# Optimization experiments

Measured on AMD Instinct MI355X. Metric: run time of the kernel, lower is better.

The kernel has to match this reference:

```python
import jax, jax.numpy as jnp
import numpy as np

N = 100000
E = 1600000
IN_C = 128
OUT_C = 64
HID = 2 * OUT_C  # 128


def setup_inputs() -> dict:
    key = jax.random.key(0)
    ks = jax.random.split(key, 10)
    s = lambda fan_in: 1.0 / np.sqrt(fan_in)
    inp = {
        "x": jax.random.normal(ks[0], (N, IN_C), dtype=jnp.float32),
        "edge_index": jax.random.randint(ks[1], (2, E), 0, N, dtype=jnp.int64),
        # SAGEConv params: lin_l acts on aggregated neighbors (with bias), lin_r on root (no bias)
        "W1l": jax.random.uniform(ks[2], (IN_C, HID), jnp.float32, -s(IN_C), s(IN_C)),
        "b1": jnp.zeros((HID,), jnp.float32),
        "W1r": jax.random.uniform(ks[3], (IN_C, HID), jnp.float32, -s(IN_C), s(IN_C)),
        "Wml": jax.random.uniform(ks[4], (HID, OUT_C), jnp.float32, -s(HID), s(HID)),
        "bm": jnp.zeros((OUT_C,), jnp.float32),
        "Wmr": jax.random.uniform(ks[5], (HID, OUT_C), jnp.float32, -s(HID), s(HID)),
        "Wsl": jax.random.uniform(ks[6], (HID, OUT_C), jnp.float32, -s(HID), s(HID)),
        "bs": jnp.zeros((OUT_C,), jnp.float32),
        "Wsr": jax.random.uniform(ks[7], (HID, OUT_C), jnp.float32, -s(HID), s(HID)),
    }
    return inp


def _sage_mean(x, src, dst, Wl, b, Wr):
    n = x.shape[0]
    # mean aggregation of source features onto destination nodes
    agg = jax.ops.segment_sum(x[src], dst, num_segments=n)
    cnt = jax.ops.segment_sum(jnp.ones((src.shape[0],), x.dtype), dst, num_segments=n)
    agg = agg / jnp.maximum(cnt, 1.0)[:, None]
    return agg @ Wl + b + x @ Wr


def reference(x, edge_index, W1l, b1, W1r, Wml, bm, Wmr, Wsl, bs, Wsr):
    src, dst = edge_index[0], edge_index[1]
    h = jax.nn.relu(_sage_mean(x, src, dst, W1l, b1, W1r))
    mu = _sage_mean(h, src, dst, Wml, bm, Wmr)
    logstd = _sage_mean(h, src, dst, Wsl, bs, Wsr)
    return mu, logstd
```

## Files before the change

### kernel.cpp

```cpp
#include <hip/hip_runtime.h>


typedef __attribute__((ext_vector_type(8))) short bf16x8;
typedef __attribute__((ext_vector_type(4))) float f32x4;
typedef __attribute__((ext_vector_type(2))) float f32x2;

#define SHIFT 9
#define BW 512

__device__ __forceinline__ unsigned short f2bf(float f) {
    unsigned u = __builtin_bit_cast(unsigned, f);
    u += 0x7fff + ((u >> 16) & 1);
    return (unsigned short)(u >> 16);
}
__device__ __forceinline__ float bflo(unsigned u) { return __builtin_bit_cast(float, u << 16); }
__device__ __forceinline__ float bfhi(unsigned u) { return __builtin_bit_cast(float, u & 0xffff0000u); }

__global__ __launch_bounds__(256) void stage1_kernel(
    const float* __restrict__ x, const int* __restrict__ raw,
    const float* __restrict__ W1l, const float* __restrict__ W1r,
    const float* __restrict__ Wml, const float* __restrict__ Wmr,
    const float* __restrict__ Wsl, const float* __restrict__ Wsr,
    const float* __restrict__ bm, const float* __restrict__ bs,
    unsigned short* __restrict__ B1p, unsigned short* __restrict__ B2p,
    float* __restrict__ bc, unsigned short* __restrict__ A1,
    unsigned short* __restrict__ A2, int* __restrict__ bcnt,
    unsigned* __restrict__ recs, int n, int nE, int cap, int nBinA, int nXB) {
    const int b = blockIdx.x;
    const int t = threadIdx.x;
    if (b < nBinA) {
        __shared__ int cnt[256];
        __shared__ int cur[256];
        __shared__ int gbase[256];
        __shared__ int sflag;
        const int e0 = b * 4096;
        const int e1 = (e0 + 4096 < nE) ? e0 + 4096 : nE;
        int acc = 0;
        for (int e = e0 + t; e < e1; e += 256) acc |= raw[2 * e + 1];
        if (t == 0) sflag = 0;
        cnt[t] = 0;
        cur[t] = 0;
        __syncthreads();
        if (acc) atomicOr(&sflag, 1);
        __syncthreads();
        const bool is64 = (sflag == 0);
        for (int e = e0 + t; e < e1; e += 256) {
            int d = is64 ? raw[2 * (nE + e)] : raw[nE + e];
            atomicAdd(&cnt[d >> SHIFT], 1);
        }
        __syncthreads();
        gbase[t] = cnt[t] ? atomicAdd(&bcnt[t], cnt[t]) : 0;
        __syncthreads();
        for (int e = e0 + t; e < e1; e += 256) {
            int s, d;
            if (is64) { s = raw[2 * e]; d = raw[2 * (nE + e)]; }
            else      { s = raw[e];     d = raw[nE + e]; }
            int bk = d >> SHIFT;
            int pos = gbase[bk] + atomicAdd(&cur[bk], 1);
            if (pos < cap)
                recs[(size_t)bk * cap + pos] = ((unsigned)s << SHIFT) | (unsigned)(d & (BW - 1));
        }
    } else if (b < nBinA + nXB) {
        int i = ((b - nBinA) * 256 + t) * 4;
        if (i < n * 128) {
            float4 v = *reinterpret_cast<const float4*>(x + i);
            int row = i >> 7, col = i & 127;
            unsigned short* p = A1 + (size_t)row * 256 + 128 + col;
            p[0] = f2bf(v.x); p[1] = f2bf(v.y); p[2] = f2bf(v.z); p[3] = f2bf(v.w);
        }
    } else if (b < nBinA + nXB + 128) {
        int i = (b - nBinA - nXB) * 256 + t;
        int j = i & 7, lq = (i >> 3) & 63, ks = (i >> 9) & 7, nf = i >> 12;
        int k = ks * 32 + (lq >> 4) * 8 + j;
        int c = nf * 16 + (lq & 15);
        float w1 = (k < 128) ? W1l[k * 128 + c] : W1r[(k - 128) * 128 + c];
        float w2;
        if (k < 128) w2 = (c < 64) ? Wml[k * 64 + c] : Wsl[k * 64 + (c - 64)];
        else         w2 = (c < 64) ? Wmr[(k - 128) * 64 + c] : Wsr[(k - 128) * 64 + (c - 64)];
        B1p[i] = f2bf(w1);
        B2p[i] = f2bf(w2);
        if (i < 128) bc[i] = (i < 64) ? bm[i] : bs[i - 64];
    } else {
        if (t < 64) {
            ((unsigned*)A1)[(size_t)n * 128 + 64 + t] = 0;
            ((unsigned*)A2)[(size_t)n * 128 + 64 + t] = 0;
        }
    }
}

__global__ __launch_bounds__(256) void binB_kernel(
    const unsigned* __restrict__ recs, const int* __restrict__ bcnt,
    int* __restrict__ rowptrP, int* __restrict__ cnts,
    int* __restrict__ csr, int cap, int n, int NB) {
    __shared__ int sdeg[BW];
    __shared__ int scur[BW];
    __shared__ int ssum[256];
    const int b = blockIdx.x;
    const int t = threadIdx.x;
    const int node0 = b << SHIFT;

    int rawb = (t < NB) ? bcnt[t] : 0;
    ssum[t] = rawb;
    __syncthreads();
    for (int off = 1; off < 256; off <<= 1) {
        int val = (t >= off) ? ssum[t - off] : 0;
        __syncthreads();
        ssum[t] += val;
        __syncthreads();
    }
    const int base = ((b == 0) ? 0 : ssum[b - 1]) + b * 3 * BW;
    int cnt = bcnt[b];
    if (cnt > cap) cnt = cap;
    const unsigned* r = recs + (size_t)b * cap;
    __syncthreads();

    sdeg[t] = 0;
    sdeg[t + 256] = 0;
    __syncthreads();
    for (int i = t; i < cnt; i += 256) atomicAdd(&sdeg[r[i] & (BW - 1)], 1);
    __syncthreads();
    int d0 = sdeg[2 * t], d1 = sdeg[2 * t + 1];
    int p0 = (d0 + 3) & ~3, p1 = (d1 + 3) & ~3;
    int sum = p0 + p1;
    ssum[t] = sum;
    __syncthreads();
    for (int off = 1; off < 256; off <<= 1) {
        int val = (t >= off) ? ssum[t - off] : 0;
        __syncthreads();
        ssum[t] += val;
        __syncthreads();
    }
    int ex = ssum[t] - sum;
    scur[2 * t] = ex;
    scur[2 * t + 1] = ex + p0;
    __syncthreads();
#pragma unroll
    for (int q = 0; q < 2; ++q) {
        int i = 2 * t + q;
        int node = node0 + i;
        if (node < n) {
            rowptrP[node] = base + scur[i];
            cnts[node] = sdeg[i];
        }
    }
    __syncthreads();
    for (int i = t; i < cnt; i += 256) {
        unsigned rec = r[i];
        int pos = base + atomicAdd(&scur[rec & (BW - 1)], 1);
        csr[pos] = (int)(rec >> SHIFT);
    }
    __syncthreads();
#pragma unroll
    for (int q = 0; q < 2; ++q) {
        int i = 2 * t + q;
        int node = node0 + i;
        if (node < n) {
            int d = sdeg[i];
            int pad = (4 - (d & 3)) & 3;
            int st = base + scur[i];
            for (int k = 0; k < pad; ++k) csr[st + k] = n;
        }
    }
}

__global__ __launch_bounds__(256) void gather_kernel(const unsigned int* __restrict__ feat,
                                                     const int* __restrict__ rowptrP,
                                                     const int* __restrict__ cnts,
                                                     const int* __restrict__ csr,
                                                     unsigned int* __restrict__ agg, int n) {
    int wv = (blockIdx.x * 256 + threadIdx.x) >> 6;
    if (wv >= n) return;
    int lane = threadIdx.x & 63;
    int eg = lane >> 4;
    int c4 = (lane & 15) * 4;
    int beg = rowptrP[wv];
    int deg = cnts[wv];
    int endp = beg + ((deg + 3) & ~3);
    f32x2 a0 = (f32x2)(0.f), a1 = (f32x2)(0.f), a2 = (f32x2)(0.f), a3 = (f32x2)(0.f);
    if (deg > 0) {
        int s0 = csr[beg + eg];
        uint4 v = *reinterpret_cast<const uint4*>(feat + (size_t)s0 * 128 + c4);
        int nx = beg + 4;
        int s1 = csr[(nx < endp ? nx : beg) + eg];
        while (nx < endp) {
            uint4 v2 = *reinterpret_cast<const uint4*>(feat + (size_t)s1 * 128 + c4);
            int nx2 = nx + 4;
            int s2 = csr[(nx2 < endp ? nx2 : beg) + eg];
            a0 += (f32x2){bflo(v.x), bfhi(v.x)};
            a1 += (f32x2){bflo(v.y), bfhi(v.y)};
            a2 += (f32x2){bflo(v.z), bfhi(v.z)};
            a3 += (f32x2){bflo(v.w), bfhi(v.w)};
            v = v2;
            s1 = s2;
            nx = nx2;
        }
        a0 += (f32x2){bflo(v.x), bfhi(v.x)};
        a1 += (f32x2){bflo(v.y), bfhi(v.y)};
        a2 += (f32x2){bflo(v.z), bfhi(v.z)};
        a3 += (f32x2){bflo(v.w), bfhi(v.w)};
    }
    float acc[8] = {a0.x, a0.y, a1.x, a1.y, a2.x, a2.y, a3.x, a3.y};
#pragma unroll
    for (int q = 0; q < 8; ++q) {
        acc[q] += __shfl_xor(acc[q], 16);
        acc[q] += __shfl_xor(acc[q], 32);
    }
    if (eg == 0) {
        float ic = 1.0f / fmaxf((float)deg, 1.0f);
        uint4 r;
        r.x = (unsigned)f2bf(acc[0] * ic) | ((unsigned)f2bf(acc[1] * ic) << 16);
        r.y = (unsigned)f2bf(acc[2] * ic) | ((unsigned)f2bf(acc[3] * ic) << 16);
        r.z = (unsigned)f2bf(acc[4] * ic) | ((unsigned)f2bf(acc[5] * ic) << 16);
        r.w = (unsigned)f2bf(acc[6] * ic) | ((unsigned)f2bf(acc[7] * ic) << 16);
        *reinterpret_cast<uint4*>(agg + (size_t)wv * 128 + c4) = r;
    }
}

template <int MODE>
__global__ __launch_bounds__(256) void mfma_gemm(const unsigned short* __restrict__ A,
                                                 const unsigned short* __restrict__ Bp,
                                                 const float* __restrict__ bias,
                                                 void* __restrict__ outp, int n) {
    const int tid = threadIdx.x;
    const int w = tid >> 6, l = tid & 63;
    const int lr = l & 15;
    const int lg = l >> 4;
    const int row0 = blockIdx.x * 128 + w * 32;

    f32x4 acc[2][8];
#pragma unroll
    for (int mf = 0; mf < 2; ++mf)
#pragma unroll
        for (int nf = 0; nf < 8; ++nf) acc[mf][nf] = (f32x4)(0.0f);

    int r0 = row0 + lr;       if (r0 > n - 1) r0 = n - 1;
    int r1 = row0 + 16 + lr;  if (r1 > n - 1) r1 = n - 1;
    const unsigned short* a0p = A + (size_t)r0 * 256 + lg * 8;
    const unsigned short* a1p = A + (size_t)r1 * 256 + lg * 8;
    const unsigned short* bp = Bp + (size_t)l * 8;

    for (int ks = 0; ks < 8; ++ks) {
        bf16x8 a0 = *reinterpret_cast<const bf16x8*>(a0p + ks * 32);
        bf16x8 a1 = *reinterpret_cast<const bf16x8*>(a1p + ks * 32);
#pragma unroll
        for (int nf = 0; nf < 8; ++nf) {
            bf16x8 b = *reinterpret_cast<const bf16x8*>(bp + ((nf * 8 + ks) << 9));
            acc[0][nf] = __builtin_amdgcn_mfma_f32_16x16x32_bf16(a0, b, acc[0][nf], 0, 0, 0);
            acc[1][nf] = __builtin_amdgcn_mfma_f32_16x16x32_bf16(a1, b, acc[1][nf], 0, 0, 0);
        }
    }

    float bv[8];
#pragma unroll
    for (int nf = 0; nf < 8; ++nf) bv[nf] = bias[nf * 16 + lr];

#pragma unroll
    for (int mf = 0; mf < 2; ++mf)
#pragma unroll
        for (int j = 0; j < 4; ++j) {
            int row = row0 + mf * 16 + lg * 4 + j;
            if (row >= n) continue;
#pragma unroll
            for (int nf = 0; nf < 8; ++nf) {
                int col = nf * 16 + lr;
                float v = acc[mf][nf][j] + bv[nf];
                if (MODE == 0) {
                    v = fmaxf(v, 0.0f);
                    ((unsigned short*)outp)[(size_t)row * 256 + 128 + col] = f2bf(v);
                } else {
                    float* o = (float*)outp;
                    if (col < 64) o[(size_t)row * 64 + col] = v;
                    else o[(size_t)n * 64 + (size_t)row * 64 + (col - 64)] = v;
                }
            }
        }
}

extern "C" void kernel_launch(void* const* d_in, const int* in_sizes, int n_in,
                              void* d_out, int out_size, void* d_ws, size_t ws_size,
                              hipStream_t stream) {
    const float* x = (const float*)d_in[0];
    const int* eidx_raw = (const int*)d_in[1];
    const float* W1l = (const float*)d_in[2];
    const float* b1 = (const float*)d_in[3];
    const float* W1r = (const float*)d_in[4];
    const float* Wml = (const float*)d_in[5];
    const float* bm = (const float*)d_in[6];
    const float* Wmr = (const float*)d_in[7];
    const float* Wsl = (const float*)d_in[8];
    const float* bs = (const float*)d_in[9];
    const float* Wsr = (const float*)d_in[10];
    float* out = (float*)d_out;

    const int n = in_sizes[0] / 128;
    const int nE = in_sizes[1] / 2;

    const int NB = ((n - 1) >> SHIFT) + 1;
    long long capll = (((long long)nE << SHIFT) / n) * 5 / 4 + 1024;
    const int cap = (int)((capll + 15) & ~15LL);
    const int csr_ints = nE + NB * 3 * BW + 64;

    char* ws = (char*)d_ws;
    const size_t a_bytes = (size_t)(n + 1) * 512;
    const size_t a1_off = 0;
    const size_t a2_off = a1_off + a_bytes;
    const size_t recs_off = a2_off;
    const size_t csr_off = a2_off + a_bytes;
    const size_t rowptr_off = csr_off + (size_t)csr_ints * 4;
    const size_t cnts_off = rowptr_off + (size_t)n * 4;
    const size_t bcnt_off = cnts_off + (size_t)n * 4;
    const size_t b1p_off = (bcnt_off + 1024 + 255) & ~(size_t)255;
    const size_t b2p_off = b1p_off + 65536;
    const size_t bc_off = b2p_off + 65536;

    unsigned short* A1 = (unsigned short*)(ws + a1_off);
    unsigned short* A2 = (unsigned short*)(ws + a2_off);
    unsigned* recs = (unsigned*)(ws + recs_off);
    int* csr = (int*)(ws + csr_off);
    int* rowptrP = (int*)(ws + rowptr_off);
    int* cnts = (int*)(ws + cnts_off);
    int* bcnt = (int*)(ws + bcnt_off);
    unsigned short* B1p = (unsigned short*)(ws + b1p_off);
    unsigned short* B2p = (unsigned short*)(ws + b2p_off);
    float* bc = (float*)(ws + bc_off);

    hipMemsetAsync(bcnt, 0, 1024, stream);

    const int nBinA = (nE + 4095) / 4096;
    const int nXB = (n * 32 + 255) / 256;
    stage1_kernel<<<nBinA + nXB + 129, 256, 0, stream>>>(
        x, eidx_raw, W1l, W1r, Wml, Wmr, Wsl, Wsr, bm, bs,
        B1p, B2p, bc, A1, A2, bcnt, recs, n, nE, cap, nBinA, nXB);

    binB_kernel<<<NB, 256, 0, stream>>>(recs, bcnt, rowptrP, cnts, csr, cap, n, NB);

    const int gather_blocks = (n * 64 + 255) / 256;
    const int gemm_blocks = (n + 127) / 128;

    gather_kernel<<<gather_blocks, 256, 0, stream>>>(
        (const unsigned int*)A1 + 64, rowptrP, cnts, csr, (unsigned int*)A1, n);
    mfma_gemm<0><<<gemm_blocks, 256, 0, stream>>>(A1, B1p, b1, A2, n);

    gather_kernel<<<gather_blocks, 256, 0, stream>>>(
        (const unsigned int*)A2 + 64, rowptrP, cnts, csr, (unsigned int*)A2, n);
    mfma_gemm<1><<<gemm_blocks, 256, 0, stream>>>(A2, B2p, bc, out, n);
}
```

Before: 269.0 us.

## Fuse neighbor gather into MFMA GEMM via LDS-staged aggregate tile

Each GEMM block now computes the mean aggregation for its own 128 rows and stores it in a swizzled LDS tile. The MFMA loop reads the aggregated half of A from LDS and the root-feature half from a compact bf16 feature array, so the aggregate no longer makes a round trip through global memory and two launches are dropped. The bucket width is halved to 256 nodes with up to 512 buckets, which doubles the binning tables. In exchange, the gather now runs with far fewer waves in flight per node (one wave walks 32 nodes serially), which may hurt latency hiding on the irregular loads.

```diff
diff --git a/kernel.cpp b/kernel.cpp
--- a/kernel.cpp
+++ b/kernel.cpp
@@ -5,8 +5,9 @@
 typedef __attribute__((ext_vector_type(4))) float f32x4;
 typedef __attribute__((ext_vector_type(2))) float f32x2;
 
-#define SHIFT 9
-#define BW 512
+#define SHIFT 8
+#define BW 256
+#define NBMAX 512
 
 __device__ __forceinline__ unsigned short f2bf(float f) {
     unsigned u = __builtin_bit_cast(unsigned, f);
@@ -23,23 +24,23 @@
     const float* __restrict__ Wsl, const float* __restrict__ Wsr,
     const float* __restrict__ bm, const float* __restrict__ bs,
     unsigned short* __restrict__ B1p, unsigned short* __restrict__ B2p,
-    float* __restrict__ bc, unsigned short* __restrict__ A1,
-    unsigned short* __restrict__ A2, int* __restrict__ bcnt,
+    float* __restrict__ bc, unsigned short* __restrict__ X16,
+    unsigned short* __restrict__ H16, int* __restrict__ bcnt,
     unsigned* __restrict__ recs, int n, int nE, int cap, int nBinA, int nXB) {
     const int b = blockIdx.x;
     const int t = threadIdx.x;
     if (b < nBinA) {
-        __shared__ int cnt[256];
-        __shared__ int cur[256];
-        __shared__ int gbase[256];
+        __shared__ int cnt[NBMAX];
+        __shared__ int cur[NBMAX];
+        __shared__ int gbase[NBMAX];
         __shared__ int sflag;
         const int e0 = b * 4096;
         const int e1 = (e0 + 4096 < nE) ? e0 + 4096 : nE;
         int acc = 0;
         for (int e = e0 + t; e < e1; e += 256) acc |= raw[2 * e + 1];
         if (t == 0) sflag = 0;
-        cnt[t] = 0;
-        cur[t] = 0;
+        cnt[t] = 0; cnt[t + 256] = 0;
+        cur[t] = 0; cur[t + 256] = 0;
         __syncthreads();
         if (acc) atomicOr(&sflag, 1);
         __syncthreads();
@@ -50,6 +51,7 @@
         }
         __syncthreads();
         gbase[t] = cnt[t] ? atomicAdd(&bcnt[t], cnt[t]) : 0;
+        gbase[t + 256] = cnt[t + 256] ? atomicAdd(&bcnt[t + 256], cnt[t + 256]) : 0;
         __syncthreads();
         for (int e = e0 + t; e < e1; e += 256) {
             int s, d;
@@ -65,7 +67,7 @@
         if (i < n * 128) {
             float4 v = *reinterpret_cast<const float4*>(x + i);
             int row = i >> 7, col = i & 127;
-            unsigned short* p = A1 + (size_t)row * 256 + 128 + col;
+            unsigned short* p = X16 + (size_t)row * 128 + col;
             p[0] = f2bf(v.x); p[1] = f2bf(v.y); p[2] = f2bf(v.z); p[3] = f2bf(v.w);
         }
     } else if (b < nBinA + nXB + 128) {
@@ -82,8 +84,8 @@
         if (i < 128) bc[i] = (i < 64) ? bm[i] : bs[i - 64];
     } else {
         if (t < 64) {
-            ((unsigned*)A1)[(size_t)n * 128 + 64 + t] = 0;
-            ((unsigned*)A2)[(size_t)n * 128 + 64 + t] = 0;
+            ((unsigned*)X16)[(size_t)n * 64 + t] = 0;
+            ((unsigned*)H16)[(size_t)n * 64 + t] = 0;
         }
     }
 }
@@ -94,54 +96,51 @@
     int* __restrict__ csr, int cap, int n, int NB) {
     __shared__ int sdeg[BW];
     __shared__ int scur[BW];
-    __shared__ int ssum[256];
+    __shared__ int sscan[256];
+    __shared__ int sb[NBMAX];
     const int b = blockIdx.x;
     const int t = threadIdx.x;
-    const int node0 = b << SHIFT;
-
-    int rawb = (t < NB) ? bcnt[t] : 0;
-    ssum[t] = rawb;
+
+    int v0 = (2 * t < NB) ? bcnt[2 * t] : 0;
+    int v1 = (2 * t + 1 < NB) ? bcnt[2 * t + 1] : 0;
+    int sum = v0 + v1;
+    sscan[t] = sum;
     __syncthreads();
     for (int off = 1; off < 256; off <<= 1) {
-        int val = (t >= off) ? ssum[t - off] : 0;
-        __syncthreads();
-        ssum[t] += val;
-        __syncthreads();
-    }
-    const int base = ((b == 0) ? 0 : ssum[b - 1]) + b * 3 * BW;
+        int val = (t >= off) ? sscan[t - off] : 0;
+        __syncthreads();
+        sscan[t] += val;
+        __syncthreads();
+    }
+    int ex = sscan[t] - sum;
+    sb[2 * t] = ex;
+    sb[2 * t + 1] = ex + v0;
+    __syncthreads();
+    const int base = sb[b] + b * 3 * BW;
     int cnt = bcnt[b];
     if (cnt > cap) cnt = cap;
     const unsigned* r = recs + (size_t)b * cap;
-    __syncthreads();
 
     sdeg[t] = 0;
-    sdeg[t + 256] = 0;
     __syncthreads();
     for (int i = t; i < cnt; i += 256) atomicAdd(&sdeg[r[i] & (BW - 1)], 1);
     __syncthreads();
-    int d0 = sdeg[2 * t], d1 = sdeg[2 * t + 1];
-    int p0 = (d0 + 3) & ~3, p1 = (d1 + 3) & ~3;
-    int sum = p0 + p1;
-    ssum[t] = sum;
+    int d = sdeg[t];
+    int p = (d + 3) & ~3;
+    sscan[t] = p;
     __syncthreads();
     for (int off = 1; off < 256; off <<= 1) {
-        int val = (t >= off) ? ssum[t - off] : 0;
-        __syncthreads();
-        ssum[t] += val;
-        __syncthreads();
-    }
-    int ex = ssum[t] - sum;
-    scur[2 * t] = ex;
-    scur[2 * t + 1] = ex + p0;
-    __syncthreads();
-#pragma unroll
-    for (int q = 0; q < 2; ++q) {
-        int i = 2 * t + q;
-        int node = node0 + i;
-        if (node < n) {
-            rowptrP[node] = base + scur[i];
-            cnts[node] = sdeg[i];
-        }
+        int val = (t >= off) ? sscan[t - off] : 0;
+        __syncthreads();
+        sscan[t] += val;
+        __syncthreads();
+    }
+    int exn = sscan[t] - p;
+    scur[t] = exn;
+    const int node = (b << SHIFT) + t;
+    if (node < n) {
+        rowptrP[node] = base + exn;
+        cnts[node] = d;
     }
     __syncthreads();
     for (int i = t; i < cnt; i += 256) {
@@ -150,79 +149,71 @@
         csr[pos] = (int)(rec >> SHIFT);
     }
     __syncthreads();
-#pragma unroll
-    for (int q = 0; q < 2; ++q) {
-        int i = 2 * t + q;
-        int node = node0 + i;
-        if (node < n) {
-            int d = sdeg[i];
-            int pad = (4 - (d & 3)) & 3;
-            int st = base + scur[i];
-            for (int k = 0; k < pad; ++k) csr[st + k] = n;
-        }
-    }
-}
-
-__global__ __launch_bounds__(256) void gather_kernel(const unsigned int* __restrict__ feat,
-                                                     const int* __restrict__ rowptrP,
-                                                     const int* __restrict__ cnts,
-                                                     const int* __restrict__ csr,
-                                                     unsigned int* __restrict__ agg, int n) {
-    int wv = (blockIdx.x * 256 + threadIdx.x) >> 6;
-    if (wv >= n) return;
-    int lane = threadIdx.x & 63;
-    int eg = lane >> 4;
-    int c4 = (lane & 15) * 4;
-    int beg = rowptrP[wv];
-    int deg = cnts[wv];
-    int endp = beg + ((deg + 3) & ~3);
-    f32x2 a0 = (f32x2)(0.f), a1 = (f32x2)(0.f), a2 = (f32x2)(0.f), a3 = (f32x2)(0.f);
-    if (deg > 0) {
-        int s0 = csr[beg + eg];
-        uint4 v = *reinterpret_cast<const uint4*>(feat + (size_t)s0 * 128 + c4);
-        int nx = beg + 4;
-        int s1 = csr[(nx < endp ? nx : beg) + eg];
-        while (nx < endp) {
-            uint4 v2 = *reinterpret_cast<const uint4*>(feat + (size_t)s1 * 128 + c4);
-            int nx2 = nx + 4;
-            int s2 = csr[(nx2 < endp ? nx2 : beg) + eg];
-            a0 += (f32x2){bflo(v.x), bfhi(v.x)};
-            a1 += (f32x2){bflo(v.y), bfhi(v.y)};
-            a2 += (f32x2){bflo(v.z), bfhi(v.z)};
-            a3 += (f32x2){bflo(v.w), bfhi(v.w)};
-            v = v2;
-            s1 = s2;
-            nx = nx2;
-        }
-        a0 += (f32x2){bflo(v.x), bfhi(v.x)};
-        a1 += (f32x2){bflo(v.y), bfhi(v.y)};
-        a2 += (f32x2){bflo(v.z), bfhi(v.z)};
-        a3 += (f32x2){bflo(v.w), bfhi(v.w)};
-    }
-    float acc[8] = {a0.x, a0.y, a1.x, a1.y, a2.x, a2.y, a3.x, a3.y};
-#pragma unroll
-    for (int q = 0; q < 8; ++q) {
-        acc[q] += __shfl_xor(acc[q], 16);
-        acc[q] += __shfl_xor(acc[q], 32);
-    }
-    if (eg == 0) {
-        float ic = 1.0f / fmaxf((float)deg, 1.0f);
-        uint4 r;
-        r.x = (unsigned)f2bf(acc[0] * ic) | ((unsigned)f2bf(acc[1] * ic) << 16);
-        r.y = (unsigned)f2bf(acc[2] * ic) | ((unsigned)f2bf(acc[3] * ic) << 16);
-        r.z = (unsigned)f2bf(acc[4] * ic) | ((unsigned)f2bf(acc[5] * ic) << 16);
-        r.w = (unsigned)f2bf(acc[6] * ic) | ((unsigned)f2bf(acc[7] * ic) << 16);
-        *reinterpret_cast<uint4*>(agg + (size_t)wv * 128 + c4) = r;
+    if (node < n) {
+        int pad = (4 - (d & 3)) & 3;
+        int st = base + scur[t];
+        for (int k = 0; k < pad; ++k) csr[st + k] = n;
     }
 }
 
 template <int MODE>
-__global__ __launch_bounds__(256) void mfma_gemm(const unsigned short* __restrict__ A,
-                                                 const unsigned short* __restrict__ Bp,
-                                                 const float* __restrict__ bias,
-                                                 void* __restrict__ outp, int n) {
+__global__ __launch_bounds__(256) void gg_kernel(
+    const unsigned short* __restrict__ feat,
+    const int* __restrict__ rowptrP, const int* __restrict__ cnts,
+    const int* __restrict__ csr, const unsigned short* __restrict__ Bp,
+    const float* __restrict__ bias, void* __restrict__ outp, int n) {
+    __shared__ __align__(16) unsigned aggT[128 * 64];
     const int tid = threadIdx.x;
     const int w = tid >> 6, l = tid & 63;
+    const unsigned* featU = (const unsigned*)feat;
+
+    {
+        const int eg = l >> 4;
+        const int c4u = (l & 15) * 4;
+        const int nodeBase = blockIdx.x * 128 + w * 32;
+        for (int i = 0; i < 32; ++i) {
+            int node = nodeBase + i;
+            if (node >= n) break;
+            int beg = rowptrP[node];
+            int deg = cnts[node];
+            int endp = beg + ((deg + 3) & ~3);
+            f32x2 a0 = (f32x2)(0.f), a1 = a0, a2 = a0, a3 = a0;
+            if (deg > 0) {
+                int s = csr[beg + eg];
+                uint4 v = *reinterpret_cast<const uint4*>(featU + (size_t)s * 64 + c4u);
+                for (int jb = beg + 4; jb < endp; jb += 4) {
+                    int s2 = csr[jb + eg];
+                    uint4 v2 = *reinterpret_cast<const uint4*>(featU + (size_t)s2 * 64 + c4u);
+                    a0 += (f32x2){bflo(v.x), bfhi(v.x)};
+                    a1 += (f32x2){bflo(v.y), bfhi(v.y)};
+                    a2 += (f32x2){bflo(v.z), bfhi(v.z)};
+                    a3 += (f32x2){bflo(v.w), bfhi(v.w)};
+                    v = v2;
+                }
+                a0 += (f32x2){bflo(v.x), bfhi(v.x)};
+                a1 += (f32x2){bflo(v.y), bfhi(v.y)};
+                a2 += (f32x2){bflo(v.z), bfhi(v.z)};
+                a3 += (f32x2){bflo(v.w), bfhi(v.w)};
+            }
+            float acc8[8] = {a0.x, a0.y, a1.x, a1.y, a2.x, a2.y, a3.x, a3.y};
+#pragma unroll
+            for (int q = 0; q < 8; ++q) {
+                acc8[q] += __shfl_xor(acc8[q], 16);
+                acc8[q] += __shfl_xor(acc8[q], 32);
+            }
+            if (eg == 0) {
+                float ic = 1.0f / fmaxf((float)deg, 1.0f);
+                uint4 r;
+                r.x = (unsigned)f2bf(acc8[0] * ic) | ((unsigned)f2bf(acc8[1] * ic) << 16);
+                r.y = (unsigned)f2bf(acc8[2] * ic) | ((unsigned)f2bf(acc8[3] * ic) << 16);
+                r.z = (unsigned)f2bf(acc8[4] * ic) | ((unsigned)f2bf(acc8[5] * ic) << 16);
+                r.w = (unsigned)f2bf(acc8[6] * ic) | ((unsigned)f2bf(acc8[7] * ic) << 16);
+                int lr = w * 32 + i;
+                *reinterpret_cast<uint4*>(&aggT[lr * 64 + (c4u ^ ((lr & 7) << 2))]) = r;
+            }
+        }
+    }
+
     const int lr = l & 15;
     const int lg = l >> 4;
     const int row0 = blockIdx.x * 128 + w * 32;
@@ -235,18 +226,34 @@
 
     int r0 = row0 + lr;       if (r0 > n - 1) r0 = n - 1;
     int r1 = row0 + 16 + lr;  if (r1 > n - 1) r1 = n - 1;
-    const unsigned short* a0p = A + (size_t)r0 * 256 + lg * 8;
-    const unsigned short* a1p = A + (size_t)r1 * 256 + lg * 8;
+    const unsigned short* a0p = feat + (size_t)r0 * 128 + lg * 8;
+    const unsigned short* a1p = feat + (size_t)r1 * 128 + lg * 8;
     const unsigned short* bp = Bp + (size_t)l * 8;
-
-    for (int ks = 0; ks < 8; ++ks) {
-        bf16x8 a0 = *reinterpret_cast<const bf16x8*>(a0p + ks * 32);
-        bf16x8 a1 = *reinterpret_cast<const bf16x8*>(a1p + ks * 32);
+    const int lr0 = w * 32 + lr, lr1 = lr0 + 16;
+
+#pragma unroll
+    for (int ks = 0; ks < 4; ++ks) {
+        int c = ks * 16 + lg * 4;
+        uint4 t0 = *reinterpret_cast<const uint4*>(&aggT[lr0 * 64 + (c ^ ((lr0 & 7) << 2))]);
+        uint4 t1 = *reinterpret_cast<const uint4*>(&aggT[lr1 * 64 + (c ^ ((lr1 & 7) << 2))]);
+        bf16x8 A0 = __builtin_bit_cast(bf16x8, t0);
+        bf16x8 A1 = __builtin_bit_cast(bf16x8, t1);
 #pragma unroll
         for (int nf = 0; nf < 8; ++nf) {
             bf16x8 b = *reinterpret_cast<const bf16x8*>(bp + ((nf * 8 + ks) << 9));
-            acc[0][nf] = __builtin_amdgcn_mfma_f32_16x16x32_bf16(a0, b, acc[0][nf], 0, 0, 0);
-            acc[1][nf] = __builtin_amdgcn_mfma_f32_16x16x32_bf16(a1, b, acc[1][nf], 0, 0, 0);
+            acc[0][nf] = __builtin_amdgcn_mfma_f32_16x16x32_bf16(A0, b, acc[0][nf], 0, 0, 0);
+            acc[1][nf] = __builtin_amdgcn_mfma_f32_16x16x32_bf16(A1, b, acc[1][nf], 0, 0, 0);
+        }
+    }
+#pragma unroll
+    for (int ks = 4; ks < 8; ++ks) {
+        bf16x8 A0 = *reinterpret_cast<const bf16x8*>(a0p + (ks - 4) * 32);
+        bf16x8 A1 = *reinterpret_cast<const bf16x8*>(a1p + (ks - 4) * 32);
+#pragma unroll
+        for (int nf = 0; nf < 8; ++nf) {
+            bf16x8 b = *reinterpret_cast<const bf16x8*>(bp + ((nf * 8 + ks) << 9));
+            acc[0][nf] = __builtin_amdgcn_mfma_f32_16x16x32_bf16(A0, b, acc[0][nf], 0, 0, 0);
+            acc[1][nf] = __builtin_amdgcn_mfma_f32_16x16x32_bf16(A1, b, acc[1][nf], 0, 0, 0);
         }
     }
 
@@ -266,7 +273,7 @@
                 float v = acc[mf][nf][j] + bv[nf];
                 if (MODE == 0) {
                     v = fmaxf(v, 0.0f);
-                    ((unsigned short*)outp)[(size_t)row * 256 + 128 + col] = f2bf(v);
+                    ((unsigned short*)outp)[(size_t)row * 128 + col] = f2bf(v);
                 } else {
                     float* o = (float*)outp;
                     if (col < 64) o[(size_t)row * 64 + col] = v;
@@ -301,20 +308,20 @@
     const int csr_ints = nE + NB * 3 * BW + 64;
 
     char* ws = (char*)d_ws;
-    const size_t a_bytes = (size_t)(n + 1) * 512;
-    const size_t a1_off = 0;
-    const size_t a2_off = a1_off + a_bytes;
-    const size_t recs_off = a2_off;
-    const size_t csr_off = a2_off + a_bytes;
+    const size_t f_bytes = (size_t)(n + 1) * 256;
+    const size_t x16_off = 0;
+    const size_t h16_off = x16_off + f_bytes;
+    const size_t recs_off = h16_off;
+    const size_t csr_off = h16_off + f_bytes;
     const size_t rowptr_off = csr_off + (size_t)csr_ints * 4;
     const size_t cnts_off = rowptr_off + (size_t)n * 4;
     const size_t bcnt_off = cnts_off + (size_t)n * 4;
-    const size_t b1p_off = (bcnt_off + 1024 + 255) & ~(size_t)255;
+    const size_t b1p_off = (bcnt_off + 2048 + 255) & ~(size_t)255;
     const size_t b2p_off = b1p_off + 65536;
     const size_t bc_off = b2p_off + 65536;
 
-    unsigned short* A1 = (unsigned short*)(ws + a1_off);
-    unsigned short* A2 = (unsigned short*)(ws + a2_off);
+    unsigned short* X16 = (unsigned short*)(ws + x16_off);
+    unsigned short* H16 = (unsigned short*)(ws + h16_off);
     unsigned* recs = (unsigned*)(ws + recs_off);
     int* csr = (int*)(ws + csr_off);
     int* rowptrP = (int*)(ws + rowptr_off);
@@ -324,24 +331,19 @@
     unsigned short* B2p = (unsigned short*)(ws + b2p_off);
     float* bc = (float*)(ws + bc_off);
 
-    hipMemsetAsync(bcnt, 0, 1024, stream);
+    hipMemsetAsync(bcnt, 0, 2048, stream);
 
     const int nBinA = (nE + 4095) / 4096;
     const int nXB = (n * 32 + 255) / 256;
     stage1_kernel<<<nBinA + nXB + 129, 256, 0, stream>>>(
         x, eidx_raw, W1l, W1r, Wml, Wmr, Wsl, Wsr, bm, bs,
-        B1p, B2p, bc, A1, A2, bcnt, recs, n, nE, cap, nBinA, nXB);
+        B1p, B2p, bc, X16, H16, bcnt, recs, n, nE, cap, nBinA, nXB);
 
     binB_kernel<<<NB, 256, 0, stream>>>(recs, bcnt, rowptrP, cnts, csr, cap, n, NB);
 
-    const int gather_blocks = (n * 64 + 255) / 256;
-    const int gemm_blocks = (n + 127) / 128;
-
-    gather_kernel<<<gather_blocks, 256, 0, stream>>>(
-        (const unsigned int*)A1 + 64, rowptrP, cnts, csr, (unsigned int*)A1, n);
-    mfma_gemm<0><<<gemm_blocks, 256, 0, stream>>>(A1, B1p, b1, A2, n);
-
-    gather_kernel<<<gather_blocks, 256, 0, stream>>>(
-        (const unsigned int*)A2 + 64, rowptrP, cnts, csr, (unsigned int*)A2, n);
-    mfma_gemm<1><<<gemm_blocks, 256, 0, stream>>>(A2, B2p, bc, out, n);
-}
+    const int gg_blocks = (n + 127) / 128;
+
+    gg_kernel<0><<<gg_blocks, 256, 0, stream>>>(X16, rowptrP, cnts, csr, B1p, b1, H16, n);
+
+    gg_kernel<1><<<gg_blocks, 256, 0, stream>>>(H16, rowptrP, cnts, csr, B2p, bc, out, n);
+}
```

After: 435.6 us. 61.9% more time.
